# Kernel optimization log

Measured on AMD Instinct MI355X. Metric: run time of the kernel, lower is better.

Reference implementation:

```python
import jax, jax.numpy as jnp
import numpy as np

N = 256          # waveguide_dims
ITERN = 3        # iter_num
B = 8192         # batch
INDEX_END = 10   # MNIST classes
ALPHA = 0.1
G = 0.05 * np.pi
PHI_B = np.pi


def setup_inputs() -> dict:
    key = jax.random.key(0)
    k1, k2, k3, k4, k5 = jax.random.split(key, 5)
    two_pi = 2.0 * np.pi
    return {
        "x_real": jax.random.normal(k1, (B, N), dtype=jnp.float32),
        "x_imag": jax.random.normal(k2, (B, N), dtype=jnp.float32),
        "theta": jax.random.uniform(k3, (ITERN, N, N // 2), dtype=jnp.float32) * two_pi,
        "phi":   jax.random.uniform(k4, (ITERN, N, N // 2), dtype=jnp.float32) * two_pi,
        "gamma": jax.random.uniform(k5, (ITERN, N), dtype=jnp.float32) * two_pi,
    }


def _mzi_mesh(x, theta, phi, gamma):
    """Rectangular (Clements) MZI mesh: N layers of 2x2 rotations + output phases.
    x: [B, N] complex64; theta, phi: [N, N//2]; gamma: [N]."""
    L = theta.shape[0]
    shifts = jnp.arange(L) % 2                      # even/odd layer offset
    full = jnp.ones((N // 2,), dtype=bool)
    odd = full.at[-1].set(False)                    # wrap-around pair inactive on odd layers
    masks = jnp.where((shifts == 1)[:, None], odd[None, :], full[None, :])

    def step(xc, inp):
        th, ph, sh, mk = inp
        xr = jnp.roll(xc, -sh, axis=1).reshape(-1, N // 2, 2)
        x0, x1 = xr[..., 0], xr[..., 1]
        half = 0.5 * th
        s, c = jnp.sin(half), jnp.cos(half)
        pre = 1j * jnp.exp(1j * half)               # common MZI prefactor
        ep = jnp.exp(1j * ph)
        y0 = pre * (ep * s * x0 + c * x1)
        y1 = pre * (ep * c * x0 - s * x1)
        y0 = jnp.where(mk, y0, x0)
        y1 = jnp.where(mk, y1, x1)
        y = jnp.stack([y0, y1], axis=-1).reshape(-1, N)
        return jnp.roll(y, sh, axis=1), None

    x, _ = jax.lax.scan(step, x, (theta, phi, shifts, masks))
    return x * jnp.exp(1j * gamma)[None, :]


def _eo_nonlin(x):
    # phase = 0.5*g*|x|^2 + 0.5*phi_b ; out = sqrt(1-alpha)*cos(phase)*exp(-i phase)*x
    phase = 0.5 * G * (x.real ** 2 + x.imag ** 2) + 0.5 * PHI_B
    return np.float32(np.sqrt(1.0 - ALPHA)) * jnp.cos(phase) * jnp.exp(-1j * phase) * x


def reference(x_real, x_imag, theta, phi, gamma):
    x = x_real.astype(jnp.complex64) + 1j * x_imag.astype(jnp.complex64)
    for i in range(ITERN):
        x = _mzi_mesh(x, theta[i], phi[i], gamma[i])
        if i != ITERN - 1:
            x = _eo_nonlin(x)
    intensity = x.real ** 2 + x.imag ** 2            # cnormsq
    norm = jnp.sqrt(jnp.sum(intensity ** 2, axis=1, keepdims=True))
    intensity = intensity / jnp.maximum(norm, 1e-12)  # F.normalize(dim=1)
    return intensity[:, :INDEX_END]
```

## Files before the change

kernel.cpp:

```cpp
#include <hip/hip_runtime.h>
#include <math.h>

#define NWG 256
#define NPAIR 128
#define NITER 3
#define NBATCH 8192
#define KDIM 512
#define MSZ (512*512)

typedef __attribute__((ext_vector_type(8))) short short8;
typedef __attribute__((ext_vector_type(4))) float floatx4;

static __device__ __forceinline__ unsigned short f2bf(float f) {
    unsigned int u = __float_as_uint(f);
    unsigned int r = (u + 0x7fffu + ((u >> 16) & 1u)) >> 16;
    return (unsigned short)r;
}
static __device__ __forceinline__ float bf2f(unsigned short h) {
    return __uint_as_float(((unsigned int)h) << 16);
}
static __device__ __forceinline__ void bsplit(float v, unsigned short &h, unsigned short &l) {
    h = f2bf(v);
    l = f2bf(v - bf2f(h));
}
static __device__ __forceinline__ void async16(const void* g, void* l) {
    __builtin_amdgcn_global_load_lds(
        (const __attribute__((address_space(1))) unsigned int*)g,
        (__attribute__((address_space(3))) unsigned int*)l, 16, 0, 0);
}

static __device__ __forceinline__ void apply2(
    float &x0r, float &x0i, float &x1r, float &x1i,
    const float4 a, const float4 b)
{
    float y0r = a.x*x0r - a.y*x0i + a.z*x1r - a.w*x1i;
    float y0i = a.x*x0i + a.y*x0r + a.z*x1i + a.w*x1r;
    float y1r = b.x*x0r - b.y*x0i + b.z*x1r - b.w*x1i;
    float y1i = b.x*x0i + b.y*x0r + b.z*x1i + b.w*x1r;
    x0r = y0r; x0i = y0i; x1r = y1r; x1i = y1i;
}

__global__ void precompute_kernel(const float* __restrict__ theta,
                                  const float* __restrict__ phi,
                                  const float* __restrict__ gamma,
                                  float* __restrict__ coef,
                                  float* __restrict__ coefT,
                                  float* __restrict__ gexp)
{
    int idx = blockIdx.x * blockDim.x + threadIdx.x;
    if (idx < NITER * NWG * NPAIR) {
        float h  = 0.5f * theta[idx];
        float ph = phi[idx];
        float sh = sinf(h),  ch = cosf(h);
        float sp = sinf(ph), cp = cosf(ph);
        float pr = -sh, pii = ch;
        float qr = pr*cp - pii*sp;
        float qi = pr*sp + pii*cp;
        float Ar = qr*sh,  Ai = qi*sh;
        float Br = pr*ch,  Bi = pii*ch;
        float Cr = qr*ch,  Ci = qi*ch;
        float Dr = -pr*sh, Di = -pii*sh;
        float4* o = (float4*)coef + (size_t)idx * 2;
        o[0] = make_float4(Ar,Ai,Br,Bi);
        o[1] = make_float4(Cr,Ci,Dr,Di);
        float4* ot = (float4*)coefT + (size_t)idx * 2;
        ot[0] = make_float4(Ar,Ai,Cr,Ci);
        ot[1] = make_float4(Br,Bi,Dr,Di);
    }
    if (idx < NITER * NWG) {
        float g = gamma[idx];
        gexp[idx*2]   = cosf(g);
        gexp[idx*2+1] = sinf(g);
    }
}

__global__ void propagate_kernel(const float* __restrict__ coef,
                                 const float* __restrict__ coefT,
                                 const float* __restrict__ gexp,
                                 unsigned short* __restrict__ chunkH,
                                 unsigned short* __restrict__ chunkL)
{
    const int lane = threadIdx.x & 63;
    const int wv   = threadIdx.x >> 6;
    const int grp  = blockIdx.x >> 6;
    const int it   = grp >> 2, c = grp & 3;
    const int row  = (blockIdx.x & 63) * 4 + wv;
    const bool rev = (c & 1);
    const bool cj  = (c == 1) || (c == 2);

    float xr[4], xi[4];
    float gc = 1.0f, gs = 0.0f;
    if (c == 3) { gc = gexp[(it*NWG + row)*2]; gs = gexp[(it*NWG + row)*2 + 1]; }
#pragma unroll
    for (int e = 0; e < 4; ++e) {
        bool on = (4*lane + e) == row;
        xr[e] = on ? gc : 0.0f;
        xi[e] = on ? gs : 0.0f;
    }

    const float4* cb = (const float4*)(rev ? coefT : coef)
                     + ((size_t)(it*NWG + c*64) * NPAIR) * 2;
    int sp0 = rev ? 63 : 0;
    const float4* p = cb + ((size_t)sp0 * NPAIR + 2*lane) * 2;
    float4 c0a = p[0], c0b = p[1], c1a = p[2], c1b = p[3];

    for (int s = 0; s < 64; ++s) {
        int sn  = (s + 1 < 64) ? s + 1 : s;
        int spn = rev ? 63 - sn : sn;
        const float4* np = cb + ((size_t)spn * NPAIR + 2*lane) * 2;
        float4 n0a = np[0], n0b = np[1], n1a = np[2], n1b = np[3];

        int sp = rev ? 63 - s : s;
        if ((sp & 1) == 0) {
            apply2(xr[0], xi[0], xr[1], xi[1], c0a, c0b);
            apply2(xr[2], xi[2], xr[3], xi[3], c1a, c1b);
        } else {
            float tr = __shfl_down(xr[0], 1, 64);
            float ti = __shfl_down(xi[0], 1, 64);
            apply2(xr[1], xi[1], xr[2], xi[2], c0a, c0b);
            float x3r = xr[3], x3i = xi[3];
            float y3r = c1a.x*x3r - c1a.y*x3i + c1a.z*tr - c1a.w*ti;
            float y3i = c1a.x*x3i + c1a.y*x3r + c1a.z*ti + c1a.w*tr;
            float ynr = c1b.x*x3r - c1b.y*x3i + c1b.z*tr - c1b.w*ti;
            float yni = c1b.x*x3i + c1b.y*x3r + c1b.z*ti + c1b.w*tr;
            float rr = __shfl_up(ynr, 1, 64);
            float ri = __shfl_up(yni, 1, 64);
            if (lane != 63) { xr[3] = y3r; xi[3] = y3i; }
            if (lane != 0)  { xr[0] = rr;  xi[0] = ri; }
        }
        c0a = n0a; c0b = n0b; c1a = n1a; c1b = n1b;
    }

    unsigned short* bh = chunkH + (size_t)grp * MSZ;
    unsigned short* bl = chunkL + (size_t)grp * MSZ;
    ushort4 reH, reL, imH, imL, nimH, nimL;
    unsigned short h, l;
#pragma unroll
    for (int e = 0; e < 4; ++e) {
        bsplit(xr[e], h, l);  ((unsigned short*)&reH)[e]  = h; ((unsigned short*)&reL)[e]  = l;
        bsplit(xi[e], h, l);  ((unsigned short*)&imH)[e]  = h; ((unsigned short*)&imL)[e]  = l;
        bsplit(-xi[e], h, l); ((unsigned short*)&nimH)[e] = h; ((unsigned short*)&nimL)[e] = l;
    }
    ushort4 urH = cj ? imH : nimH, urL = cj ? imL : nimL;
    ushort4 llH = cj ? nimH : imH, llL = cj ? nimL : imL;
    *(ushort4*)(bh + (size_t)row*KDIM + 4*lane)             = reH;
    *(ushort4*)(bh + (size_t)row*KDIM + 256 + 4*lane)       = urH;
    *(ushort4*)(bh + (size_t)(row+256)*KDIM + 4*lane)       = llH;
    *(ushort4*)(bh + (size_t)(row+256)*KDIM + 256 + 4*lane) = reH;
    *(ushort4*)(bl + (size_t)row*KDIM + 4*lane)             = reL;
    *(ushort4*)(bl + (size_t)row*KDIM + 256 + 4*lane)       = urL;
    *(ushort4*)(bl + (size_t)(row+256)*KDIM + 4*lane)       = llL;
    *(ushort4*)(bl + (size_t)(row+256)*KDIM + 256 + 4*lane) = reL;
}

__global__ __launch_bounds__(256, 2) void compose_kernel(
    const unsigned short* __restrict__ srcH, const unsigned short* __restrict__ srcL,
    unsigned short* __restrict__ outH, unsigned short* __restrict__ outL,
    unsigned short* __restrict__ bmat, int mode)
{
    __shared__ unsigned short sAh[2048], sAl[2048], sBh[2048], sBl[2048];
    const int z = blockIdx.z;
    const unsigned short *Ah, *Al, *Bh, *Bl;
    if (mode == 0) {
        int it = z >> 1, wh = z & 1;
        int ai = it*4 + (wh ? 3 : 0), bi = it*4 + (wh ? 2 : 1);
        Ah = srcH + (size_t)ai*MSZ; Al = srcL + (size_t)ai*MSZ;
        Bh = srcH + (size_t)bi*MSZ; Bl = srcL + (size_t)bi*MSZ;
    } else {
        Ah = srcH + (size_t)(2*z+1)*MSZ; Al = srcL + (size_t)(2*z+1)*MSZ;
        Bh = srcH + (size_t)(2*z)*MSZ;   Bl = srcL + (size_t)(2*z)*MSZ;
    }
    const int tid = threadIdx.x, lane = tid & 63, wv = tid >> 6;
    const int quad = lane >> 4, l16 = lane & 15;
    const int m0 = blockIdx.x * 64, n0 = blockIdx.y * 64;
    const unsigned short* src = (wv==0)?Ah:(wv==1)?Al:(wv==2)?Bh:Bl;
    unsigned short* dst = (wv==0)?sAh:(wv==1)?sAl:(wv==2)?sBh:sBl;
    const int r0 = (wv < 2) ? m0 : n0;
    const int trowb = lane >> 2, tcol = (lane & 3) * 8;

    floatx4 acc[4] = {};
    for (int kt = 0; kt < KDIM; kt += 32) {
        __syncthreads();
#pragma unroll
        for (int i = 0; i < 4; ++i)
            async16(src + (size_t)(r0 + i*16 + trowb)*KDIM + kt + tcol,
                    dst + i*512 + lane*8);
        __syncthreads();
        short8 ah = *(const short8*)&sAh[(16*wv + l16)*32 + quad*8];
        short8 al = *(const short8*)&sAl[(16*wv + l16)*32 + quad*8];
#pragma unroll
        for (int ni = 0; ni < 4; ++ni) {
            short8 bh = *(const short8*)&sBh[(16*ni + l16)*32 + quad*8];
            short8 bl = *(const short8*)&sBl[(16*ni + l16)*32 + quad*8];
            acc[ni] = __builtin_amdgcn_mfma_f32_16x16x32_bf16(ah, bh, acc[ni], 0,0,0);
            acc[ni] = __builtin_amdgcn_mfma_f32_16x16x32_bf16(ah, bl, acc[ni], 0,0,0);
            acc[ni] = __builtin_amdgcn_mfma_f32_16x16x32_bf16(al, bh, acc[ni], 0,0,0);
        }
    }
#pragma unroll
    for (int ni = 0; ni < 4; ++ni)
#pragma unroll
        for (int rg = 0; rg < 4; ++rg) {
            int r = m0 + 16*wv + quad*4 + rg;
            int cc = n0 + 16*ni + l16;
            float v = acc[ni][rg];
            if (mode == 0) {
                float vs = (((z & 1) == 0) && ((r >= 256) != (cc >= 256))) ? -v : v;
                unsigned short h, l; bsplit(vs, h, l);
                outH[(size_t)z*MSZ + (size_t)r*KDIM + cc] = h;
                outL[(size_t)z*MSZ + (size_t)r*KDIM + cc] = l;
            } else {
                bmat[(size_t)z*MSZ + (size_t)r*KDIM + cc] = f2bf(v);
            }
        }
}

__global__ void convert_kernel(const float* __restrict__ xre,
                               const float* __restrict__ xim,
                               unsigned short* __restrict__ xb)
{
    int idx = blockIdx.x * 256 + threadIdx.x;
    int b = idx >> 8, j = idx & 255;
    xb[(size_t)b * KDIM + j]       = f2bf(xre[idx]);
    xb[(size_t)b * KDIM + 256 + j] = f2bf(xim[idx]);
}

__global__ __launch_bounds__(256, 2) void gemm_kernel(
    const unsigned short* __restrict__ A, const unsigned short* __restrict__ Bm,
    int mode, unsigned short* __restrict__ xout, float* __restrict__ Iout)
{
    __shared__ unsigned short sA[64*32];
    __shared__ unsigned short sB[128*32];
    const int tid = threadIdx.x, lane = tid & 63, wv = tid >> 6;
    const int quad = lane >> 4, l16 = lane & 15;
    const int m0 = blockIdx.x * 64, n0 = blockIdx.y * 64;
    const int trowb = lane >> 2, tcol = (lane & 3) * 8;

    floatx4 acc[8] = {};
    for (int kt = 0; kt < KDIM; kt += 32) {
        __syncthreads();
        async16(A + (size_t)(m0 + 16*wv + trowb)*KDIM + kt + tcol,
                &sA[wv*512 + lane*8]);
#pragma unroll
        for (int j = 0; j < 2; ++j) {
            int trow = 32*wv + 16*j + trowb;
            int grow = (trow < 64) ? (n0 + trow) : (n0 + trow + 192);
            async16(Bm + (size_t)grow*KDIM + kt + tcol,
                    &sB[(32*wv + 16*j)*32 + lane*8]);
        }
        __syncthreads();
        short8 a = *(const short8*)&sA[(16*wv + l16)*32 + quad*8];
#pragma unroll
        for (int ni = 0; ni < 8; ++ni) {
            short8 b = *(const short8*)&sB[(16*ni + l16)*32 + quad*8];
            acc[ni] = __builtin_amdgcn_mfma_f32_16x16x32_bf16(a, b, acc[ni], 0,0,0);
        }
    }
#pragma unroll
    for (int ni = 0; ni < 4; ++ni)
#pragma unroll
        for (int rg = 0; rg < 4; ++rg) {
            int row = m0 + 16*wv + quad*4 + rg;
            int cc  = n0 + 16*ni + l16;
            float yr = acc[ni][rg], yi = acc[ni+4][rg];
            if (mode == 2) {
                Iout[(size_t)row*256 + cc] = yr*yr + yi*yi;
            } else {
                float I = yr*yr + yi*yi;
                float phase = 0.078539816339744831f * I + 1.5707963267948966f;
                float sp, cp; __sincosf(phase, &sp, &cp);
                float f = 0.94868329805051381f * cp;
                xout[(size_t)row*KDIM + cc]       = f2bf(f*(cp*yr + sp*yi));
                xout[(size_t)row*KDIM + cc + 256] = f2bf(f*(cp*yi - sp*yr));
            }
        }
}

__global__ void final_kernel(const float* __restrict__ Ibuf,
                             float* __restrict__ out)
{
    const int lane = threadIdx.x & 63;
    const int wv   = threadIdx.x >> 6;
    const int row  = blockIdx.x * 4 + wv;
    float4 v = *(const float4*)(Ibuf + (size_t)row * 256 + 4*lane);
    float ss = v.x*v.x + v.y*v.y + v.z*v.z + v.w*v.w;
#pragma unroll
    for (int d = 1; d < 64; d <<= 1) ss += __shfl_xor(ss, d, 64);
    float inv = 1.0f / fmaxf(sqrtf(ss), 1e-12f);
    float* o = out + (size_t)row * 10;
    if (lane == 0)      { o[0]=v.x*inv; o[1]=v.y*inv; o[2]=v.z*inv; o[3]=v.w*inv; }
    else if (lane == 1) { o[4]=v.x*inv; o[5]=v.y*inv; o[6]=v.z*inv; o[7]=v.w*inv; }
    else if (lane == 2) { o[8]=v.x*inv; o[9]=v.y*inv; }
}

extern "C" void kernel_launch(void* const* d_in, const int* in_sizes, int n_in,
                              void* d_out, int out_size, void* d_ws, size_t ws_size,
                              hipStream_t stream)
{
    const float* x_real = (const float*)d_in[0];
    const float* x_imag = (const float*)d_in[1];
    const float* theta  = (const float*)d_in[2];
    const float* phi    = (const float*)d_in[3];
    const float* gamma  = (const float*)d_in[4];

    char* ws = (char*)d_ws;
    float* coef  = (float*)(ws + 0);
    float* coefT = (float*)(ws + 3145728);
    float* gexp  = (float*)(ws + 6291456);
    unsigned short* chunkH = (unsigned short*)(ws + 6297600);
    unsigned short* chunkL = (unsigned short*)(ws + 12589056);
    unsigned short* PH   = (unsigned short*)(ws + 0);
    unsigned short* PL   = (unsigned short*)(ws + 3145728);
    unsigned short* xbuf0 = (unsigned short*)(ws + 6297600);
    unsigned short* xbuf1 = (unsigned short*)(ws + 14686208);
    float* Ibuf = (float*)(ws + 14686208);
    unsigned short* Bmat = (unsigned short*)(ws + 23074816);

    precompute_kernel<<<(NITER*NWG*NPAIR + 255)/256, 256, 0, stream>>>(
        theta, phi, gamma, coef, coefT, gexp);

    propagate_kernel<<<768, 256, 0, stream>>>(coef, coefT, gexp, chunkH, chunkL);

    compose_kernel<<<dim3(8,8,6), 256, 0, stream>>>(chunkH, chunkL, PH, PL, Bmat, 0);
    compose_kernel<<<dim3(8,8,3), 256, 0, stream>>>(PH, PL, PH, PL, Bmat, 1);

    convert_kernel<<<NBATCH*NWG/256, 256, 0, stream>>>(x_real, x_imag, xbuf0);

    gemm_kernel<<<dim3(128,4), 256, 0, stream>>>(xbuf0, Bmat,           0, xbuf1, (float*)nullptr);
    gemm_kernel<<<dim3(128,4), 256, 0, stream>>>(xbuf1, Bmat + MSZ,     1, xbuf0, (float*)nullptr);
    gemm_kernel<<<dim3(128,4), 256, 0, stream>>>(xbuf0, Bmat + 2*MSZ,   2, (unsigned short*)nullptr, Ibuf);

    final_kernel<<<NBATCH/4, 256, 0, stream>>>(Ibuf, (float*)d_out);
}
```

Measured before the change: 191.1 us.

## Split mesh into eight chunks, store compact complex planes, fuse input conversion

The MZI mesh propagation now uses eight 32-layer chunks per iteration instead of four 64-layer chunks. This doubles the number of propagation blocks and halves the serial depth each one runs. Chunk products are kept as compact 256x256 real/imag planes rather than the 512x512 real-block embedding, and compose rebuilds the block structure with sign flips while loading. The last compose level expands the result into the real GEMM matrix. The transposed coefficient array is dropped (swizzled in registers instead), and the fp32-to-bf16 input conversion is folded into the propagation launch as extra blocks. In exchange there is one more compose launch and the global_load_lds async copies are replaced by synchronous loads in compose.

```diff
diff --git a/kernel.cpp b/kernel.cpp
--- a/kernel.cpp
+++ b/kernel.cpp
@@ -7,6 +7,11 @@
 #define NBATCH 8192
 #define KDIM 512
 #define MSZ (512*512)
+#define PLANE 65536
+#define CMSZ (2*PLANE)
+#define NCHUNK 8
+#define CHL 32
+#define PROPBLK 1536
 
 typedef __attribute__((ext_vector_type(8))) short short8;
 typedef __attribute__((ext_vector_type(4))) float floatx4;
@@ -44,7 +49,6 @@
                                   const float* __restrict__ phi,
                                   const float* __restrict__ gamma,
                                   float* __restrict__ coef,
-                                  float* __restrict__ coefT,
                                   float* __restrict__ gexp)
 {
     int idx = blockIdx.x * blockDim.x + threadIdx.x;
@@ -56,16 +60,9 @@
         float pr = -sh, pii = ch;
         float qr = pr*cp - pii*sp;
         float qi = pr*sp + pii*cp;
-        float Ar = qr*sh,  Ai = qi*sh;
-        float Br = pr*ch,  Bi = pii*ch;
-        float Cr = qr*ch,  Ci = qi*ch;
-        float Dr = -pr*sh, Di = -pii*sh;
         float4* o = (float4*)coef + (size_t)idx * 2;
-        o[0] = make_float4(Ar,Ai,Br,Bi);
-        o[1] = make_float4(Cr,Ci,Dr,Di);
-        float4* ot = (float4*)coefT + (size_t)idx * 2;
-        ot[0] = make_float4(Ar,Ai,Cr,Ci);
-        ot[1] = make_float4(Br,Bi,Dr,Di);
+        o[0] = make_float4(qr*sh,  qi*sh,  pr*ch,  pii*ch);
+        o[1] = make_float4(qr*ch,  qi*ch, -pr*sh, -pii*sh);
     }
     if (idx < NITER * NWG) {
         float g = gamma[idx];
@@ -74,23 +71,32 @@
     }
 }
 
-__global__ void propagate_kernel(const float* __restrict__ coef,
-                                 const float* __restrict__ coefT,
+__global__ void prop_conv_kernel(const float* __restrict__ coef,
                                  const float* __restrict__ gexp,
+                                 const float* __restrict__ xre,
+                                 const float* __restrict__ xim,
                                  unsigned short* __restrict__ chunkH,
-                                 unsigned short* __restrict__ chunkL)
-{
+                                 unsigned short* __restrict__ chunkL,
+                                 unsigned short* __restrict__ xb)
+{
+    if (blockIdx.x >= PROPBLK) {
+        int idx = (blockIdx.x - PROPBLK) * 256 + threadIdx.x;
+        int b = idx >> 8, j = idx & 255;
+        xb[(size_t)b * KDIM + j]       = f2bf(xre[idx]);
+        xb[(size_t)b * KDIM + 256 + j] = f2bf(xim[idx]);
+        return;
+    }
+
     const int lane = threadIdx.x & 63;
     const int wv   = threadIdx.x >> 6;
     const int grp  = blockIdx.x >> 6;
-    const int it   = grp >> 2, c = grp & 3;
+    const int it   = grp >> 3, c = grp & 7;
     const int row  = (blockIdx.x & 63) * 4 + wv;
     const bool rev = (c & 1);
-    const bool cj  = (c == 1) || (c == 2);
 
     float xr[4], xi[4];
     float gc = 1.0f, gs = 0.0f;
-    if (c == 3) { gc = gexp[(it*NWG + row)*2]; gs = gexp[(it*NWG + row)*2 + 1]; }
+    if (c == 7) { gc = gexp[(it*NWG + row)*2]; gs = gexp[(it*NWG + row)*2 + 1]; }
 #pragma unroll
     for (int e = 0; e < 4; ++e) {
         bool on = (4*lane + e) == row;
@@ -98,31 +104,40 @@
         xi[e] = on ? gs : 0.0f;
     }
 
-    const float4* cb = (const float4*)(rev ? coefT : coef)
-                     + ((size_t)(it*NWG + c*64) * NPAIR) * 2;
-    int sp0 = rev ? 63 : 0;
+    const float4* cb = (const float4*)coef + ((size_t)(it*NWG + c*CHL) * NPAIR) * 2;
+    int sp0 = rev ? CHL-1 : 0;
     const float4* p = cb + ((size_t)sp0 * NPAIR + 2*lane) * 2;
     float4 c0a = p[0], c0b = p[1], c1a = p[2], c1b = p[3];
 
-    for (int s = 0; s < 64; ++s) {
-        int sn  = (s + 1 < 64) ? s + 1 : s;
-        int spn = rev ? 63 - sn : sn;
+    for (int s = 0; s < CHL; ++s) {
+        int sn  = (s + 1 < CHL) ? s + 1 : s;
+        int spn = rev ? CHL-1 - sn : sn;
         const float4* np = cb + ((size_t)spn * NPAIR + 2*lane) * 2;
         float4 n0a = np[0], n0b = np[1], n1a = np[2], n1b = np[3];
 
-        int sp = rev ? 63 - s : s;
+        float4 u0a, u0b, u1a, u1b;
+        if (rev) {
+            u0a = make_float4(c0a.x, c0a.y, c0b.x, c0b.y);
+            u0b = make_float4(c0a.z, c0a.w, c0b.z, c0b.w);
+            u1a = make_float4(c1a.x, c1a.y, c1b.x, c1b.y);
+            u1b = make_float4(c1a.z, c1a.w, c1b.z, c1b.w);
+        } else {
+            u0a = c0a; u0b = c0b; u1a = c1a; u1b = c1b;
+        }
+
+        int sp = rev ? CHL-1 - s : s;
         if ((sp & 1) == 0) {
-            apply2(xr[0], xi[0], xr[1], xi[1], c0a, c0b);
-            apply2(xr[2], xi[2], xr[3], xi[3], c1a, c1b);
+            apply2(xr[0], xi[0], xr[1], xi[1], u0a, u0b);
+            apply2(xr[2], xi[2], xr[3], xi[3], u1a, u1b);
         } else {
             float tr = __shfl_down(xr[0], 1, 64);
             float ti = __shfl_down(xi[0], 1, 64);
-            apply2(xr[1], xi[1], xr[2], xi[2], c0a, c0b);
+            apply2(xr[1], xi[1], xr[2], xi[2], u0a, u0b);
             float x3r = xr[3], x3i = xi[3];
-            float y3r = c1a.x*x3r - c1a.y*x3i + c1a.z*tr - c1a.w*ti;
-            float y3i = c1a.x*x3i + c1a.y*x3r + c1a.z*ti + c1a.w*tr;
-            float ynr = c1b.x*x3r - c1b.y*x3i + c1b.z*tr - c1b.w*ti;
-            float yni = c1b.x*x3i + c1b.y*x3r + c1b.z*ti + c1b.w*tr;
+            float y3r = u1a.x*x3r - u1a.y*x3i + u1a.z*tr - u1a.w*ti;
+            float y3i = u1a.x*x3i + u1a.y*x3r + u1a.z*ti + u1a.w*tr;
+            float ynr = u1b.x*x3r - u1b.y*x3i + u1b.z*tr - u1b.w*ti;
+            float yni = u1b.x*x3i + u1b.y*x3r + u1b.z*ti + u1b.w*tr;
             float rr = __shfl_up(ynr, 1, 64);
             float ri = __shfl_up(yni, 1, 64);
             if (lane != 63) { xr[3] = y3r; xi[3] = y3i; }
@@ -131,61 +146,70 @@
         c0a = n0a; c0b = n0b; c1a = n1a; c1b = n1b;
     }
 
-    unsigned short* bh = chunkH + (size_t)grp * MSZ;
-    unsigned short* bl = chunkL + (size_t)grp * MSZ;
-    ushort4 reH, reL, imH, imL, nimH, nimL;
+    unsigned short* bh = chunkH + (size_t)grp * CMSZ;
+    unsigned short* bl = chunkL + (size_t)grp * CMSZ;
+    ushort4 reH, reL, imH, imL;
     unsigned short h, l;
 #pragma unroll
     for (int e = 0; e < 4; ++e) {
-        bsplit(xr[e], h, l);  ((unsigned short*)&reH)[e]  = h; ((unsigned short*)&reL)[e]  = l;
-        bsplit(xi[e], h, l);  ((unsigned short*)&imH)[e]  = h; ((unsigned short*)&imL)[e]  = l;
-        bsplit(-xi[e], h, l); ((unsigned short*)&nimH)[e] = h; ((unsigned short*)&nimL)[e] = l;
-    }
-    ushort4 urH = cj ? imH : nimH, urL = cj ? imL : nimL;
-    ushort4 llH = cj ? nimH : imH, llL = cj ? nimL : imL;
-    *(ushort4*)(bh + (size_t)row*KDIM + 4*lane)             = reH;
-    *(ushort4*)(bh + (size_t)row*KDIM + 256 + 4*lane)       = urH;
-    *(ushort4*)(bh + (size_t)(row+256)*KDIM + 4*lane)       = llH;
-    *(ushort4*)(bh + (size_t)(row+256)*KDIM + 256 + 4*lane) = reH;
-    *(ushort4*)(bl + (size_t)row*KDIM + 4*lane)             = reL;
-    *(ushort4*)(bl + (size_t)row*KDIM + 256 + 4*lane)       = urL;
-    *(ushort4*)(bl + (size_t)(row+256)*KDIM + 4*lane)       = llL;
-    *(ushort4*)(bl + (size_t)(row+256)*KDIM + 256 + 4*lane) = reL;
+        bsplit(xr[e], h, l); ((unsigned short*)&reH)[e] = h; ((unsigned short*)&reL)[e] = l;
+        bsplit(xi[e], h, l); ((unsigned short*)&imH)[e] = h; ((unsigned short*)&imL)[e] = l;
+    }
+    *(ushort4*)(bh + (size_t)row*256 + 4*lane)         = reH;
+    *(ushort4*)(bh + PLANE + (size_t)row*256 + 4*lane) = imH;
+    *(ushort4*)(bl + (size_t)row*256 + 4*lane)         = reL;
+    *(ushort4*)(bl + PLANE + (size_t)row*256 + 4*lane) = imL;
 }
 
 __global__ __launch_bounds__(256, 2) void compose_kernel(
     const unsigned short* __restrict__ srcH, const unsigned short* __restrict__ srcL,
     unsigned short* __restrict__ outH, unsigned short* __restrict__ outL,
-    unsigned short* __restrict__ bmat, int mode)
+    unsigned short* __restrict__ bmat, int level)
 {
     __shared__ unsigned short sAh[2048], sAl[2048], sBh[2048], sBl[2048];
     const int z = blockIdx.z;
-    const unsigned short *Ah, *Al, *Bh, *Bl;
-    if (mode == 0) {
+    int ai, bi;
+    if (level == 0) {
+        const int amap[4] = {0,3,4,7}, bmap[4] = {1,2,5,6};
+        int it = z >> 2, j = z & 3;
+        ai = it*NCHUNK + amap[j]; bi = it*NCHUNK + bmap[j];
+    } else if (level == 1) {
         int it = z >> 1, wh = z & 1;
-        int ai = it*4 + (wh ? 3 : 0), bi = it*4 + (wh ? 2 : 1);
-        Ah = srcH + (size_t)ai*MSZ; Al = srcL + (size_t)ai*MSZ;
-        Bh = srcH + (size_t)bi*MSZ; Bl = srcL + (size_t)bi*MSZ;
+        ai = it*4 + (wh ? 3 : 0); bi = it*4 + (wh ? 2 : 1);
     } else {
-        Ah = srcH + (size_t)(2*z+1)*MSZ; Al = srcL + (size_t)(2*z+1)*MSZ;
-        Bh = srcH + (size_t)(2*z)*MSZ;   Bl = srcL + (size_t)(2*z)*MSZ;
+        ai = 2*z + 1; bi = 2*z;
     }
     const int tid = threadIdx.x, lane = tid & 63, wv = tid >> 6;
     const int quad = lane >> 4, l16 = lane & 15;
-    const int m0 = blockIdx.x * 64, n0 = blockIdx.y * 64;
-    const unsigned short* src = (wv==0)?Ah:(wv==1)?Al:(wv==2)?Bh:Bl;
+    const int m0 = blockIdx.x * 64;
+    const int n0 = blockIdx.y * 64;
+    const bool isA = (wv < 2);
+    const unsigned short* mat = ((wv & 1) ? srcL : srcH) + (size_t)(isA ? ai : bi) * CMSZ;
     unsigned short* dst = (wv==0)?sAh:(wv==1)?sAl:(wv==2)?sBh:sBl;
-    const int r0 = (wv < 2) ? m0 : n0;
-    const int trowb = lane >> 2, tcol = (lane & 3) * 8;
+    const int l2 = lane >> 2, kq = (lane & 3) * 8;
+    const int rowb = isA ? ((m0 < 256) ? m0 : m0 - 256) : n0;
 
     floatx4 acc[4] = {};
     for (int kt = 0; kt < KDIM; kt += 32) {
+        int po; bool neg = false;
+        if (kt < 256) po = (isA && m0 >= 256) ? PLANE : 0;
+        else {
+            if (isA) { if (m0 < 256) { po = PLANE; neg = true; } else po = 0; }
+            else po = PLANE;
+        }
+        int keff = (kt < 256 ? kt : kt - 256) + kq;
+        const unsigned short* sp_ = mat + po;
+
         __syncthreads();
 #pragma unroll
-        for (int i = 0; i < 4; ++i)
-            async16(src + (size_t)(r0 + i*16 + trowb)*KDIM + kt + tcol,
-                    dst + i*512 + lane*8);
+        for (int i = 0; i < 4; ++i) {
+            int rl = i*16 + l2;
+            uint4 v = *(const uint4*)(sp_ + (size_t)(rowb + rl)*256 + keff);
+            if (neg) { v.x ^= 0x80008000u; v.y ^= 0x80008000u; v.z ^= 0x80008000u; v.w ^= 0x80008000u; }
+            *(uint4*)(dst + rl*32 + kq) = v;
+        }
         __syncthreads();
+
         short8 ah = *(const short8*)&sAh[(16*wv + l16)*32 + quad*8];
         short8 al = *(const short8*)&sAl[(16*wv + l16)*32 + quad*8];
 #pragma unroll
@@ -204,25 +228,23 @@
             int r = m0 + 16*wv + quad*4 + rg;
             int cc = n0 + 16*ni + l16;
             float v = acc[ni][rg];
-            if (mode == 0) {
-                float vs = (((z & 1) == 0) && ((r >= 256) != (cc >= 256))) ? -v : v;
-                unsigned short h, l; bsplit(vs, h, l);
-                outH[(size_t)z*MSZ + (size_t)r*KDIM + cc] = h;
-                outL[(size_t)z*MSZ + (size_t)r*KDIM + cc] = l;
+            if (level < 2) {
+                unsigned short h, l; bsplit(v, h, l);
+                size_t off = (size_t)z*CMSZ + ((r < 256) ? ((size_t)r*256 + cc)
+                                                         : (PLANE + (size_t)(r-256)*256 + cc));
+                outH[off] = h; outL[off] = l;
             } else {
-                bmat[(size_t)z*MSZ + (size_t)r*KDIM + cc] = f2bf(v);
+                unsigned short* bm = bmat + (size_t)z*MSZ;
+                if (r < 256) {
+                    unsigned short h = f2bf(v);
+                    bm[(size_t)r*KDIM + cc] = h;
+                    bm[(size_t)(r+256)*KDIM + cc + 256] = h;
+                } else {
+                    bm[(size_t)r*KDIM + cc] = f2bf(v);
+                    bm[(size_t)(r-256)*KDIM + cc + 256] = f2bf(-v);
+                }
             }
         }
-}
-
-__global__ void convert_kernel(const float* __restrict__ xre,
-                               const float* __restrict__ xim,
-                               unsigned short* __restrict__ xb)
-{
-    int idx = blockIdx.x * 256 + threadIdx.x;
-    int b = idx >> 8, j = idx & 255;
-    xb[(size_t)b * KDIM + j]       = f2bf(xre[idx]);
-    xb[(size_t)b * KDIM + 256 + j] = f2bf(xim[idx]);
 }
 
 __global__ __launch_bounds__(256, 2) void gemm_kernel(
@@ -305,30 +327,31 @@
 
     char* ws = (char*)d_ws;
     float* coef  = (float*)(ws + 0);
-    float* coefT = (float*)(ws + 3145728);
-    float* gexp  = (float*)(ws + 6291456);
-    unsigned short* chunkH = (unsigned short*)(ws + 6297600);
-    unsigned short* chunkL = (unsigned short*)(ws + 12589056);
-    unsigned short* PH   = (unsigned short*)(ws + 0);
-    unsigned short* PL   = (unsigned short*)(ws + 3145728);
-    unsigned short* xbuf0 = (unsigned short*)(ws + 6297600);
-    unsigned short* xbuf1 = (unsigned short*)(ws + 14686208);
-    float* Ibuf = (float*)(ws + 14686208);
-    unsigned short* Bmat = (unsigned short*)(ws + 23074816);
+    float* gexp  = (float*)(ws + 3145728);
+    unsigned short* chunkH = (unsigned short*)(ws + 3153920);
+    unsigned short* chunkL = (unsigned short*)(ws + 9445376);
+    unsigned short* TL     = (unsigned short*)(ws + 15736832);
+    unsigned short* xbuf0  = (unsigned short*)(ws + 18882560);
+    unsigned short* TH     = (unsigned short*)(ws + 0);
+    unsigned short* PH     = (unsigned short*)(ws + 3153920);
+    unsigned short* PL     = (unsigned short*)(ws + 4726784);
+    unsigned short* bmat   = (unsigned short*)(ws + 6299648);
+    unsigned short* xbuf1  = (unsigned short*)(ws + 7872512);
+    float* Ibuf            = (float*)(ws + 7872512);
 
     precompute_kernel<<<(NITER*NWG*NPAIR + 255)/256, 256, 0, stream>>>(
-        theta, phi, gamma, coef, coefT, gexp);
-
-    propagate_kernel<<<768, 256, 0, stream>>>(coef, coefT, gexp, chunkH, chunkL);
-
-    compose_kernel<<<dim3(8,8,6), 256, 0, stream>>>(chunkH, chunkL, PH, PL, Bmat, 0);
-    compose_kernel<<<dim3(8,8,3), 256, 0, stream>>>(PH, PL, PH, PL, Bmat, 1);
-
-    convert_kernel<<<NBATCH*NWG/256, 256, 0, stream>>>(x_real, x_imag, xbuf0);
-
-    gemm_kernel<<<dim3(128,4), 256, 0, stream>>>(xbuf0, Bmat,           0, xbuf1, (float*)nullptr);
-    gemm_kernel<<<dim3(128,4), 256, 0, stream>>>(xbuf1, Bmat + MSZ,     1, xbuf0, (float*)nullptr);
-    gemm_kernel<<<dim3(128,4), 256, 0, stream>>>(xbuf0, Bmat + 2*MSZ,   2, (unsigned short*)nullptr, Ibuf);
+        theta, phi, gamma, coef, gexp);
+
+    prop_conv_kernel<<<PROPBLK + NBATCH*NWG/256, 256, 0, stream>>>(
+        coef, gexp, x_real, x_imag, chunkH, chunkL, xbuf0);
+
+    compose_kernel<<<dim3(8,4,12), 256, 0, stream>>>(chunkH, chunkL, TH, TL, nullptr, 0);
+    compose_kernel<<<dim3(8,4,6),  256, 0, stream>>>(TH, TL, PH, PL, nullptr, 1);
+    compose_kernel<<<dim3(8,4,3),  256, 0, stream>>>(PH, PL, nullptr, nullptr, bmat, 2);
+
+    gemm_kernel<<<dim3(128,4), 256, 0, stream>>>(xbuf0, bmat,           0, xbuf1, (float*)nullptr);
+    gemm_kernel<<<dim3(128,4), 256, 0, stream>>>(xbuf1, bmat + MSZ,     1, xbuf0, (float*)nullptr);
+    gemm_kernel<<<dim3(128,4), 256, 0, stream>>>(xbuf0, bmat + 2*MSZ,   2, (unsigned short*)nullptr, Ibuf);
 
     final_kernel<<<NBATCH/4, 256, 0, stream>>>(Ibuf, (float*)d_out);
 }
```

Result: slower. 229.3 us (+20.0%).
